# Performance work log

Hardware: AMD Instinct MI355X
Metric: run time of the kernel (lower is better)

The kernel has to match this reference:

```python
import jax, jax.numpy as jnp
import numpy as np

D_MODEL = 1024
N_HEADS = 16
D_HEAD = D_MODEL // N_HEADS
ROPE_THETA = 10000.0


def apply_rope(x, positions):
    # x: [b, h, s, d], positions: [s]
    half = x.shape[-1] // 2
    inv_freq = ROPE_THETA ** (-jnp.arange(half, dtype=x.dtype) * 2.0 / x.shape[-1])
    ang = positions.astype(x.dtype)[:, None] * inv_freq[None, :]  # [s, half]
    cos, sin = jnp.cos(ang), jnp.sin(ang)
    x1, x2 = x[..., 0::2], x[..., 1::2]  # rotate interleaved pairs (x_{2k}, x_{2k+1})
    out_even = x1 * cos - x2 * sin
    out_odd = x1 * sin + x2 * cos
    return jnp.stack([out_even, out_odd], axis=-1).reshape(x.shape)


def setup_inputs() -> dict:
    key = jax.random.key(0)
    k1, k2, k3 = jax.random.split(key, 3)
    b, s = 4, 2048
    x = jax.random.normal(k1, (b, s, D_MODEL), dtype=jnp.float32)
    w_qkv = jax.random.normal(k2, (3 * D_MODEL, D_MODEL), dtype=jnp.float32) * (D_MODEL ** -0.5)
    w_out = jax.random.normal(k3, (D_MODEL, D_MODEL), dtype=jnp.float32) * (D_MODEL ** -0.5)
    return {"x": x, "w_qkv": w_qkv, "w_out": w_out}


def reference(x, w_qkv, w_out):
    b, s, _ = x.shape
    qkv = jnp.einsum('bsd,ed->bse', x, w_qkv)  # fused QKV projection
    qkv = qkv.reshape(b, s, 3, N_HEADS, D_HEAD).transpose(2, 0, 3, 1, 4)  # [3, b, h, s, d]
    q, k, v = qkv[0], qkv[1], qkv[2]
    positions = jnp.arange(s)
    q = apply_rope(q, positions)
    k = apply_rope(k, positions)
    scale = 1.0 / np.sqrt(D_HEAD)
    scores = jnp.einsum('bhqd,bhkd->bhqk', q, k) * scale
    causal = jnp.tril(jnp.ones((s, s), dtype=bool))
    scores = jnp.where(causal, scores, jnp.finfo(scores.dtype).min)
    attn = jax.nn.softmax(scores, axis=-1)
    out = jnp.einsum('bhqk,bhkd->bhqd', attn, v)
    out = out.transpose(0, 2, 1, 3).reshape(b, s, D_MODEL)  # b h s d -> b s (h d)
    return jnp.einsum('bsd,ed->bse', out, w_out)
```

## Files before the change

### kernel.cpp

```cpp
#include <hip/hip_runtime.h>
#include <math.h>

#define D_MODEL 1024
#define NH      16
#define DH      64
#define S_LEN   2048
#define BATCH   4

typedef unsigned short u16;
typedef __attribute__((ext_vector_type(8))) short s8v;
typedef __attribute__((ext_vector_type(4))) float f4v;

#define MFMA(a, b, c) __builtin_amdgcn_mfma_f32_16x16x32_bf16((a), (b), (c), 0, 0, 0)

__device__ inline u16 f2bf(float f) {
  unsigned u = __float_as_uint(f);
  u += 0x7fffu + ((u >> 16) & 1u);
  return (u16)(u >> 16);
}
__device__ inline float bf2f(u16 h) {
  return __uint_as_float(((unsigned)h) << 16);
}
__device__ inline u16 f2bf_trunc(float f) {
  return (u16)(__float_as_uint(f) >> 16);
}
__device__ inline void split4(const float4 v, short4& h4, short4& l4) {
  u16 hx = f2bf(v.x), hy = f2bf(v.y), hz = f2bf(v.z), hw = f2bf(v.w);
  h4 = make_short4((short)hx, (short)hy, (short)hz, (short)hw);
  l4 = make_short4((short)f2bf_trunc(v.x - bf2f(hx)), (short)f2bf_trunc(v.y - bf2f(hy)),
                   (short)f2bf_trunc(v.z - bf2f(hz)), (short)f2bf_trunc(v.w - bf2f(hw)));
}

__global__ void rope_table_kernel(float* __restrict__ tab) {
  int i = blockIdx.x * 256 + threadIdx.x;
  if (i >= S_LEN * 32) return;
  int s = i >> 5;
  int p = i & 31;
  float invf = (float)pow(10000.0, -(double)p / 32.0);
  float ang = (float)s * invf;
  tab[i]         = cosf(ang);
  tab[65536 + i] = sinf(ang);
}

__global__ __launch_bounds__(256) void split_kernel(
    const float* __restrict__ src, u16* __restrict__ dh, u16* __restrict__ dl, int n4) {
  int i = blockIdx.x * 256 + threadIdx.x;
  if (i >= n4) return;
  float4 v = reinterpret_cast<const float4*>(src)[i];
  short4 h4, l4;
  split4(v, h4, l4);
  reinterpret_cast<short4*>(dh)[i] = h4;
  reinterpret_cast<short4*>(dl)[i] = l4;
}

template <int MODE>
__global__ __launch_bounds__(256) void gemm2(
    const u16* __restrict__ Ah, const u16* __restrict__ Al,
    const u16* __restrict__ Bh, const u16* __restrict__ Bl,
    float* __restrict__ C,
    u16* __restrict__ qh, u16* __restrict__ ql,
    u16* __restrict__ kh, u16* __restrict__ kl,
    float* __restrict__ vw,
    const float* __restrict__ tab,
    int M, int N, int K)
{
  __shared__ u16 As[2][128][40];
  __shared__ u16 Bs[2][128][40];

  const int tid  = threadIdx.x;
  const int lane = tid & 63;
  const int wave = tid >> 6;
  const int wm = wave >> 1, wn = wave & 1;
  const int m0 = blockIdx.y * 128;
  const int n0 = blockIdx.x * 128;

  const int lr = lane & 15;
  const int lk = (lane >> 4) * 8;

  const int srow = tid >> 1;
  const int skc  = (tid & 1) * 16;

  f4v acc[4][4] = {};

  s8v ra[2][2], rb[2][2];
  {
    const size_t ab = (size_t)(m0 + srow) * K + skc;
    const size_t bb = (size_t)(n0 + srow) * K + skc;
    ra[0][0] = *(const s8v*)(Ah + ab);  ra[0][1] = *(const s8v*)(Ah + ab + 8);
    ra[1][0] = *(const s8v*)(Al + ab);  ra[1][1] = *(const s8v*)(Al + ab + 8);
    rb[0][0] = *(const s8v*)(Bh + bb);  rb[0][1] = *(const s8v*)(Bh + bb + 8);
    rb[1][0] = *(const s8v*)(Bl + bb);  rb[1][1] = *(const s8v*)(Bl + bb + 8);
  }

  for (int k0 = 0; k0 < K; k0 += 32) {
    __syncthreads();
    *(s8v*)&As[0][srow][skc] = ra[0][0];  *(s8v*)&As[0][srow][skc + 8] = ra[0][1];
    *(s8v*)&As[1][srow][skc] = ra[1][0];  *(s8v*)&As[1][srow][skc + 8] = ra[1][1];
    *(s8v*)&Bs[0][srow][skc] = rb[0][0];  *(s8v*)&Bs[0][srow][skc + 8] = rb[0][1];
    *(s8v*)&Bs[1][srow][skc] = rb[1][0];  *(s8v*)&Bs[1][srow][skc + 8] = rb[1][1];
    __syncthreads();

    if (k0 + 32 < K) {
      const size_t ab = (size_t)(m0 + srow) * K + k0 + 32 + skc;
      const size_t bb = (size_t)(n0 + srow) * K + k0 + 32 + skc;
      ra[0][0] = *(const s8v*)(Ah + ab);  ra[0][1] = *(const s8v*)(Ah + ab + 8);
      ra[1][0] = *(const s8v*)(Al + ab);  ra[1][1] = *(const s8v*)(Al + ab + 8);
      rb[0][0] = *(const s8v*)(Bh + bb);  rb[0][1] = *(const s8v*)(Bh + bb + 8);
      rb[1][0] = *(const s8v*)(Bl + bb);  rb[1][1] = *(const s8v*)(Bl + bb + 8);
    }

    s8v ah[4], al[4], bh[4], bl[4];
#pragma unroll
    for (int x = 0; x < 4; ++x) {
      ah[x] = *(const s8v*)&As[0][wm * 64 + x * 16 + lr][lk];
      al[x] = *(const s8v*)&As[1][wm * 64 + x * 16 + lr][lk];
      bh[x] = *(const s8v*)&Bs[0][wn * 64 + x * 16 + lr][lk];
      bl[x] = *(const s8v*)&Bs[1][wn * 64 + x * 16 + lr][lk];
    }
#pragma unroll
    for (int mf = 0; mf < 4; ++mf)
#pragma unroll
      for (int nf = 0; nf < 4; ++nf) {
        acc[mf][nf] = MFMA(ah[mf], bh[nf], acc[mf][nf]);
        acc[mf][nf] = MFMA(al[mf], bh[nf], acc[mf][nf]);
        acc[mf][nf] = MFMA(ah[mf], bl[nf], acc[mf][nf]);
      }
  }

  if (MODE == 0) {
#pragma unroll
    for (int mf = 0; mf < 4; ++mf)
#pragma unroll
      for (int nf = 0; nf < 4; ++nf) {
        int c = n0 + wn * 64 + nf * 16 + lr;
#pragma unroll
        for (int i = 0; i < 4; ++i) {
          int m = m0 + wm * 64 + mf * 16 + (lane >> 4) * 4 + i;
          C[(size_t)m * N + c] = acc[mf][nf][i];
        }
      }
  } else {
#pragma unroll
    for (int nf = 0; nf < 4; ++nf) {
      int c = n0 + wn * 64 + nf * 16 + lr;
      int t = c >> 10;
      int h = (c & 1023) >> 6;
      int d = c & 63;
#pragma unroll
      for (int mf = 0; mf < 4; ++mf)
#pragma unroll
        for (int i = 0; i < 4; ++i) {
          int m = m0 + wm * 64 + mf * 16 + (lane >> 4) * 4 + i;
          int b = m >> 11, s = m & 2047;
          float v  = acc[mf][nf][i];
          float pv = __shfl_xor(v, 1);
          size_t off = ((size_t)(b * NH + h) * S_LEN + s) * DH + d;
          if (t == 2) {
            vw[off] = v;
          } else {
            int p = d >> 1;
            float co = tab[s * 32 + p], si = tab[65536 + s * 32 + p];
            float res = ((d & 1) == 0) ? (v * co - pv * si)
                                       : (pv * si + v * co);
            u16 hi = f2bf(res);
            u16 lo = f2bf_trunc(res - bf2f(hi));
            ((t == 0) ? qh : kh)[off] = hi;
            ((t == 0) ? ql : kl)[off] = lo;
          }
        }
    }
  }
}

__global__ __launch_bounds__(256) void vtrans_kernel(
    const float* __restrict__ vw, u16* __restrict__ vth)
{
  __shared__ float T[64][65];
  const int tid = threadIdx.x;
  const int st = blockIdx.x, bh = blockIdx.y;
  const int s0 = st * 64;
#pragma unroll
  for (int it = 0; it < 4; ++it) {
    int f = it * 256 + tid;
    int r = f >> 4, c4 = (f & 15) * 4;
    float4 v = *(const float4*)&vw[((size_t)bh * S_LEN + s0 + r) * DH + c4];
    T[r][c4 + 0] = v.x; T[r][c4 + 1] = v.y; T[r][c4 + 2] = v.z; T[r][c4 + 3] = v.w;
  }
  __syncthreads();
#pragma unroll
  for (int it = 0; it < 16; ++it) {
    int f = it * 256 + tid;
    int d = f >> 6, sc = f & 63;
    vth[((size_t)bh * DH + d) * S_LEN + s0 + sc] = f2bf(T[sc][d]);
  }
}

__global__ __launch_bounds__(256) void attn4_kernel(
    const u16* __restrict__ qhp, const u16* __restrict__ qlp,
    const u16* __restrict__ khp, const u16* __restrict__ klp,
    const u16* __restrict__ vthp,
    u16* __restrict__ ohp, u16* __restrict__ olp)
{
  __shared__ u16 Kh[64][72], Kl[64][72];
  __shared__ u16 Vh[64][72];
  __shared__ u16 Ph[4][16][72];

  const int tid  = threadIdx.x;
  const int lane = tid & 63;
  const int w    = tid >> 6;
  const int bid = blockIdx.x;
  const int swz = (bid & 7) * 256 + (bid >> 3);
  const int bh  = swz >> 5;
  const int qt  = 31 - (swz & 31);
  const int q0  = qt * 64;

  const int lr = lane & 15;
  const int lk = (lane >> 4) * 8;
  const int rg = (lane >> 4) * 4;

  const size_t kvbase = (size_t)bh * S_LEN * DH;
  const size_t vtbase = (size_t)bh * DH * S_LEN;

  const int sr  = tid >> 2;
  const int sc0 = (tid & 3) * 16;

  const u16* qrow_h = qhp + kvbase + (size_t)(q0 + w * 16 + lr) * DH;
  const u16* qrow_l = qlp + kvbase + (size_t)(q0 + w * 16 + lr) * DH;
  s8v qfh[2], qfl[2];
#pragma unroll
  for (int c = 0; c < 2; ++c) {
    qfh[c] = *(const s8v*)(qrow_h + c * 32 + lk);
    qfl[c] = *(const s8v*)(qrow_l + c * 32 + lk);
  }

  float m_run[4] = {-3.0e38f, -3.0e38f, -3.0e38f, -3.0e38f};
  float l_run[4] = {0.f, 0.f, 0.f, 0.f};
  f4v o[4] = {};

  s8v rkh[2], rkl[2], rvh[2];
  {
    const size_t koff = kvbase + (size_t)sr * DH + sc0;
    const size_t voff = vtbase + (size_t)sr * S_LEN + sc0;
    rkh[0] = *(const s8v*)(khp + koff);   rkh[1] = *(const s8v*)(khp + koff + 8);
    rkl[0] = *(const s8v*)(klp + koff);   rkl[1] = *(const s8v*)(klp + koff + 8);
    rvh[0] = *(const s8v*)(vthp + voff);  rvh[1] = *(const s8v*)(vthp + voff + 8);
  }

  for (int kt = 0; kt <= qt; ++kt) {
    __syncthreads();
    *(s8v*)&Kh[sr][sc0] = rkh[0];  *(s8v*)&Kh[sr][sc0 + 8] = rkh[1];
    *(s8v*)&Kl[sr][sc0] = rkl[0];  *(s8v*)&Kl[sr][sc0 + 8] = rkl[1];
    *(s8v*)&Vh[sr][sc0] = rvh[0];  *(s8v*)&Vh[sr][sc0 + 8] = rvh[1];
    __syncthreads();

    if (kt < qt) {
      const int kn = (kt + 1) * 64;
      const size_t koff = kvbase + (size_t)(kn + sr) * DH + sc0;
      const size_t voff = vtbase + (size_t)sr * S_LEN + kn + sc0;
      rkh[0] = *(const s8v*)(khp + koff);   rkh[1] = *(const s8v*)(khp + koff + 8);
      rkl[0] = *(const s8v*)(klp + koff);   rkl[1] = *(const s8v*)(klp + koff + 8);
      rvh[0] = *(const s8v*)(vthp + voff);  rvh[1] = *(const s8v*)(vthp + voff + 8);
    }

    f4v sf[4] = {};
#pragma unroll
    for (int f = 0; f < 4; ++f)
#pragma unroll
      for (int c = 0; c < 2; ++c) {
        s8v kbh = *(const s8v*)&Kh[f * 16 + lr][c * 32 + lk];
        s8v kbl = *(const s8v*)&Kl[f * 16 + lr][c * 32 + lk];
        sf[f] = MFMA(qfh[c], kbh, sf[f]);
        sf[f] = MFMA(qfl[c], kbh, sf[f]);
        sf[f] = MFMA(qfh[c], kbl, sf[f]);
      }

    const bool diag = (kt == qt);
    float p[4][4];
    float sc[4][4];
#pragma unroll
    for (int f = 0; f < 4; ++f)
#pragma unroll
      for (int i = 0; i < 4; ++i) {
        float v = sf[f][i] * 0.125f;
        if (diag) {
          int col = f * 16 + lr;
          int row = w * 16 + rg + i;
          if (col > row) v = -3.0e38f;
        }
        sc[f][i] = v;
      }
#pragma unroll
    for (int i = 0; i < 4; ++i) {
      float mx = fmaxf(fmaxf(sc[0][i], sc[1][i]), fmaxf(sc[2][i], sc[3][i]));
#pragma unroll
      for (int off = 1; off < 16; off <<= 1) mx = fmaxf(mx, __shfl_xor(mx, off));
      float mnew  = fmaxf(m_run[i], mx);
      float alpha = __expf(m_run[i] - mnew);
      float rs = 0.f;
#pragma unroll
      for (int f = 0; f < 4; ++f) { p[f][i] = __expf(sc[f][i] - mnew); rs += p[f][i]; }
#pragma unroll
      for (int off = 1; off < 16; off <<= 1) rs += __shfl_xor(rs, off);
      l_run[i] = l_run[i] * alpha + rs;
      m_run[i] = mnew;
#pragma unroll
      for (int f2 = 0; f2 < 4; ++f2) o[f2][i] *= alpha;
    }

#pragma unroll
    for (int f = 0; f < 4; ++f)
#pragma unroll
      for (int i = 0; i < 4; ++i)
        Ph[w][rg + i][f * 16 + lr] = f2bf(p[f][i]);

#pragma unroll
    for (int c = 0; c < 2; ++c) {
      s8v pah = *(const s8v*)&Ph[w][lr][c * 32 + lk];
#pragma unroll
      for (int f2 = 0; f2 < 4; ++f2) {
        s8v vbh = *(const s8v*)&Vh[f2 * 16 + lr][c * 32 + lk];
        o[f2] = MFMA(pah, vbh, o[f2]);
      }
    }
  }

  const int b = bh >> 4, h = bh & 15;
#pragma unroll
  for (int i = 0; i < 4; ++i) {
    int s = q0 + w * 16 + rg + i;
    float inv = 1.0f / l_run[i];
#pragma unroll
    for (int f2 = 0; f2 < 4; ++f2) {
      int d = f2 * 16 + lr;
      float val = o[f2][i] * inv;
      size_t off = ((size_t)(b * S_LEN + s)) * D_MODEL + h * DH + d;
      u16 hi = f2bf(val);
      ohp[off] = hi;
      olp[off] = f2bf_trunc(val - bf2f(hi));
    }
  }
}

extern "C" void kernel_launch(void* const* d_in, const int* in_sizes, int n_in,
                              void* d_out, int out_size, void* d_ws, size_t ws_size,
                              hipStream_t stream) {
  const float* x     = (const float*)d_in[0];
  const float* w_qkv = (const float*)d_in[1];
  const float* w_out = (const float*)d_in[2];
  float* out = (float*)d_out;

  const size_t NQ = (size_t)BATCH * NH * S_LEN * DH;
  const size_t NWQ = (size_t)3 * D_MODEL * D_MODEL;
  const size_t NWO = (size_t)D_MODEL * D_MODEL;

  float* ws  = (float*)d_ws;
  float* tab = ws;
  float* vw  = ws + 131072;
  u16* u   = (u16*)(vw + NQ);
  u16* xh  = u;  u += NQ;
  u16* xl  = u;  u += NQ;
  u16* wqh = u;  u += NWQ;
  u16* wql = u;  u += NWQ;
  u16* woh = u;  u += NWO;
  u16* wol = u;  u += NWO;
  u16* qh  = u;  u += NQ;
  u16* ql  = u;  u += NQ;
  u16* kh  = u;  u += NQ;
  u16* kl  = u;  u += NQ;
  u16* vth = u;  u += NQ;

  const int M = BATCH * S_LEN;

  rope_table_kernel<<<(S_LEN * 32 + 255) / 256, 256, 0, stream>>>(tab);

  split_kernel<<<(int)(NQ / 4 + 255) / 256, 256, 0, stream>>>(x, xh, xl, (int)(NQ / 4));
  split_kernel<<<(int)(NWQ / 4 + 255) / 256, 256, 0, stream>>>(w_qkv, wqh, wql, (int)(NWQ / 4));
  split_kernel<<<(int)(NWO / 4 + 255) / 256, 256, 0, stream>>>(w_out, woh, wol, (int)(NWO / 4));

  gemm2<1><<<dim3(3 * D_MODEL / 128, M / 128), 256, 0, stream>>>(
      xh, xl, wqh, wql, nullptr, qh, ql, kh, kl, vw, tab, M, 3 * D_MODEL, D_MODEL);

  vtrans_kernel<<<dim3(S_LEN / 64, BATCH * NH), 256, 0, stream>>>(vw, vth);

  u16* oh = xh;
  u16* ol = xl;
  attn4_kernel<<<dim3(S_LEN / 64 * BATCH * NH), 256, 0, stream>>>(
      qh, ql, kh, kl, vth, oh, ol);

  gemm2<0><<<dim3(D_MODEL / 128, M / 128), 256, 0, stream>>>(
      oh, ol, woh, wol, out, nullptr, nullptr, nullptr, nullptr, nullptr, tab,
      M, D_MODEL, D_MODEL);
}
```

Before: 548.6 us.

## Load GEMM tiles directly into LDS with global_load_lds, drop register prefetch

Both GEMMs now copy A and B tiles from global memory straight into shared memory with the direct-to-LDS load builtin, instead of staging them through registers. The shared tiles lose their padding (row stride 32 instead of 40) so the copy layout matches. The register-based prefetch of the next k-tile is removed, so each iteration loads, waits for vmcnt(0) and then computes with no overlap. The unpadded layout may also cause LDS bank conflicts on the fragment reads.

```diff
diff --git a/kernel.cpp b/kernel.cpp
--- a/kernel.cpp
+++ b/kernel.cpp
@@ -12,6 +12,11 @@
 typedef __attribute__((ext_vector_type(4))) float f4v;
 
 #define MFMA(a, b, c) __builtin_amdgcn_mfma_f32_16x16x32_bf16((a), (b), (c), 0, 0, 0)
+
+#define GLOAD16(g, l)                                                        \
+  __builtin_amdgcn_global_load_lds(                                          \
+      (const __attribute__((address_space(1))) void*)(g),                    \
+      (__attribute__((address_space(3))) void*)(l), 16, 0, 0)
 
 __device__ inline u16 f2bf(float f) {
   unsigned u = __float_as_uint(f);
@@ -54,7 +59,7 @@
 }
 
 template <int MODE>
-__global__ __launch_bounds__(256) void gemm2(
+__global__ __launch_bounds__(256) void gemm3(
     const u16* __restrict__ Ah, const u16* __restrict__ Al,
     const u16* __restrict__ Bh, const u16* __restrict__ Bl,
     float* __restrict__ C,
@@ -64,50 +69,38 @@
     const float* __restrict__ tab,
     int M, int N, int K)
 {
-  __shared__ u16 As[2][128][40];
-  __shared__ u16 Bs[2][128][40];
+  __shared__ u16 As[2][128][32];
+  __shared__ u16 Bs[2][128][32];
 
   const int tid  = threadIdx.x;
   const int lane = tid & 63;
-  const int wave = tid >> 6;
-  const int wm = wave >> 1, wn = wave & 1;
+  const int wv   = tid >> 6;
+  const int wm = wv >> 1, wn = wv & 1;
   const int m0 = blockIdx.y * 128;
   const int n0 = blockIdx.x * 128;
 
   const int lr = lane & 15;
   const int lk = (lane >> 4) * 8;
 
-  const int srow = tid >> 1;
-  const int skc  = (tid & 1) * 16;
+  const int gr = lane >> 2;
+  const int gc = (lane & 3) * 8;
 
   f4v acc[4][4] = {};
-
-  s8v ra[2][2], rb[2][2];
-  {
-    const size_t ab = (size_t)(m0 + srow) * K + skc;
-    const size_t bb = (size_t)(n0 + srow) * K + skc;
-    ra[0][0] = *(const s8v*)(Ah + ab);  ra[0][1] = *(const s8v*)(Ah + ab + 8);
-    ra[1][0] = *(const s8v*)(Al + ab);  ra[1][1] = *(const s8v*)(Al + ab + 8);
-    rb[0][0] = *(const s8v*)(Bh + bb);  rb[0][1] = *(const s8v*)(Bh + bb + 8);
-    rb[1][0] = *(const s8v*)(Bl + bb);  rb[1][1] = *(const s8v*)(Bl + bb + 8);
-  }
 
   for (int k0 = 0; k0 < K; k0 += 32) {
     __syncthreads();
-    *(s8v*)&As[0][srow][skc] = ra[0][0];  *(s8v*)&As[0][srow][skc + 8] = ra[0][1];
-    *(s8v*)&As[1][srow][skc] = ra[1][0];  *(s8v*)&As[1][srow][skc + 8] = ra[1][1];
-    *(s8v*)&Bs[0][srow][skc] = rb[0][0];  *(s8v*)&Bs[0][srow][skc + 8] = rb[0][1];
-    *(s8v*)&Bs[1][srow][skc] = rb[1][0];  *(s8v*)&Bs[1][srow][skc + 8] = rb[1][1];
+#pragma unroll
+    for (int j = 0; j < 2; ++j) {
+      const int r0 = wv * 32 + j * 16;
+      const size_t ga = (size_t)(m0 + r0 + gr) * K + k0 + gc;
+      const size_t gb = (size_t)(n0 + r0 + gr) * K + k0 + gc;
+      GLOAD16(Ah + ga, &As[0][r0][0]);
+      GLOAD16(Al + ga, &As[1][r0][0]);
+      GLOAD16(Bh + gb, &Bs[0][r0][0]);
+      GLOAD16(Bl + gb, &Bs[1][r0][0]);
+    }
+    asm volatile("s_waitcnt vmcnt(0)" ::: "memory");
     __syncthreads();
-
-    if (k0 + 32 < K) {
-      const size_t ab = (size_t)(m0 + srow) * K + k0 + 32 + skc;
-      const size_t bb = (size_t)(n0 + srow) * K + k0 + 32 + skc;
-      ra[0][0] = *(const s8v*)(Ah + ab);  ra[0][1] = *(const s8v*)(Ah + ab + 8);
-      ra[1][0] = *(const s8v*)(Al + ab);  ra[1][1] = *(const s8v*)(Al + ab + 8);
-      rb[0][0] = *(const s8v*)(Bh + bb);  rb[0][1] = *(const s8v*)(Bh + bb + 8);
-      rb[1][0] = *(const s8v*)(Bl + bb);  rb[1][1] = *(const s8v*)(Bl + bb + 8);
-    }
 
     s8v ah[4], al[4], bh[4], bl[4];
 #pragma unroll
@@ -377,7 +370,7 @@
   split_kernel<<<(int)(NWQ / 4 + 255) / 256, 256, 0, stream>>>(w_qkv, wqh, wql, (int)(NWQ / 4));
   split_kernel<<<(int)(NWO / 4 + 255) / 256, 256, 0, stream>>>(w_out, woh, wol, (int)(NWO / 4));
 
-  gemm2<1><<<dim3(3 * D_MODEL / 128, M / 128), 256, 0, stream>>>(
+  gemm3<1><<<dim3(3 * D_MODEL / 128, M / 128), 256, 0, stream>>>(
       xh, xl, wqh, wql, nullptr, qh, ql, kh, kl, vw, tab, M, 3 * D_MODEL, D_MODEL);
 
   vtrans_kernel<<<dim3(S_LEN / 64, BATCH * NH), 256, 0, stream>>>(vw, vth);
@@ -387,7 +380,7 @@
   attn4_kernel<<<dim3(S_LEN / 64 * BATCH * NH), 256, 0, stream>>>(
       qh, ql, kh, kl, vth, oh, ol);
 
-  gemm2<0><<<dim3(D_MODEL / 128, M / 128), 256, 0, stream>>>(
+  gemm3<0><<<dim3(D_MODEL / 128, M / 128), 256, 0, stream>>>(
       oh, ol, woh, wol, out, nullptr, nullptr, nullptr, nullptr, nullptr, tab,
       M, D_MODEL, D_MODEL);
 }
```

Result: slower. 569.8 us (+3.9%).
